# Kernel tuning notes

Measured on AMD Instinct MI355X. Metric: run time of the kernel, lower is better.

The kernel has to match this reference:

```python
import jax, jax.numpy as jnp
import numpy as np

B, N = 1, 1024
C_S, C_Z, N_HEAD, C_HEAD = 384, 128, 16, 24
HC = N_HEAD * C_HEAD


def _ln(x, eps=1e-5):
    m = jnp.mean(x, axis=-1, keepdims=True)
    v = jnp.var(x, axis=-1, keepdims=True)
    return (x - m) / jnp.sqrt(v + eps)


def setup_inputs() -> dict:
    key = jax.random.key(0)
    ks = jax.random.split(key, 24)
    w = lambda k, shp: (jax.random.normal(k, shp, jnp.float32) * 0.02)
    return {
        "a_i": jax.random.normal(ks[0], (B, N, C_S), jnp.float32),
        "s_i": jax.random.normal(ks[1], (B, N, C_S), jnp.float32),
        "z_ij": jax.random.normal(ks[2], (B, N, N, C_Z), jnp.float32),
        # AdaLN params
        "adaln_lns_w": jnp.ones((C_S,), jnp.float32),      # layer_norm_s weight (no bias)
        "adaln_ws": w(ks[3], (C_S, C_S)),                   # linear_s weight
        "adaln_bs": jnp.zeros((C_S,), jnp.float32),         # linear_s bias
        "adaln_wns": w(ks[4], (C_S, C_S)),                  # linear_no_bias_s
        # attention projections
        "wq": w(ks[5], (C_S, HC)),
        "bq": jnp.zeros((HC,), jnp.float32),
        "wk": w(ks[6], (C_S, HC)),
        "wv": w(ks[7], (C_S, HC)),
        # pair bias
        "lnb_w": jnp.ones((C_Z,), jnp.float32),
        "lnb_b": jnp.zeros((C_Z,), jnp.float32),
        "wb": w(ks[8], (C_Z, N_HEAD)),
        # gate + output
        "wg": w(ks[9], (C_S, HC)),
        "wo": w(ks[10], (HC, C_S)),
        # final conditioning gate (bias init -2.0 per module)
        "ws": w(ks[11], (C_S, C_S)),
        "bs": jnp.full((C_S,), -2.0, jnp.float32),
    }


def reference(a_i, s_i, z_ij, adaln_lns_w, adaln_ws, adaln_bs, adaln_wns,
              wq, bq, wk, wv, lnb_w, lnb_b, wb, wg, wo, ws, bs):
    b, n, _ = a_i.shape
    H, D = N_HEAD, C_HEAD
    # AdaLN: a <- sigmoid(Lin(s)) * LN(a) + Lin_nb(s)
    a = _ln(a_i)
    s = _ln(s_i) * adaln_lns_w
    a = jax.nn.sigmoid(s @ adaln_ws + adaln_bs) * a + s @ adaln_wns
    # QKV projections -> [b, i, h, d]
    q = (a @ wq + bq).reshape(b, n, H, D)
    k = (a @ wk).reshape(b, n, H, D)
    v = (a @ wv).reshape(b, n, H, D)
    # pair bias [b, h, i, j]
    bias = jnp.einsum('bijc,ch->bhij', _ln(z_ij) * lnb_w + lnb_b, wb)
    # gate [b, i, h, d]
    g = jax.nn.sigmoid(a @ wg).reshape(b, n, H, D)
    logits = jnp.einsum('bihd,bjhd->bhij', q, k) / jnp.sqrt(jnp.float32(D)) + bias
    A = jax.nn.softmax(logits, axis=-1)
    o = jnp.einsum('bhij,bjhd->bihd', A, v) * g
    o = o.reshape(b, n, H * D) @ wo
    # final gate uses raw s_i
    return jax.nn.sigmoid(s_i @ ws + bs) * o
```

## Files before the change

kernel.cpp:

```cpp
#include <hip/hip_runtime.h>
#include <hip/hip_bf16.h>
#include <math.h>

#define N_SEQ 1024
#define CS 384
#define CZ 128
#define NH 16
#define CH 24
#define HC 384

typedef float  floatx4 __attribute__((ext_vector_type(4)));
typedef short  shortx8 __attribute__((ext_vector_type(8)));
typedef unsigned int uintx4 __attribute__((ext_vector_type(4)));

__device__ __forceinline__ unsigned short f2bf(float f){
  union { float fv; unsigned u; } c; c.fv = f;
  unsigned u = c.u;
  return (unsigned short)((u + 0x7fffu + ((u >> 16) & 1u)) >> 16);
}
__device__ __forceinline__ float bf2f(unsigned short s){
  union { unsigned u; float fv; } c; c.u = ((unsigned)s) << 16; return c.fv;
}
__device__ __forceinline__ float bf_lo(unsigned u){
  union { unsigned uu; float f; } c; c.uu = u << 16; return c.f;
}
__device__ __forceinline__ float bf_hi(unsigned u){
  union { unsigned uu; float f; } c; c.uu = u & 0xffff0000u; return c.f;
}
__device__ __forceinline__ float sigmoidf_(float x){ return 1.f / (1.f + __expf(-x)); }

__device__ __forceinline__ void bias_unit(int u, int tid, int nthr,
    const float* __restrict__ z, const float* __restrict__ lnb_w,
    const float* __restrict__ lnb_b, const float* __restrict__ wb,
    unsigned short* __restrict__ bias, float (*ob)[65])
{
  int i    = u >> 4;
  int j0   = (u & 15) * 64;
  int wave = tid >> 6;
  int lane = tid & 63;

  if (wave < 4){
    int m = lane & 15;
    int q = lane >> 4;
    int jbase = j0 + wave * 16;

    shortx8 bfrag[4];
    float sumw = 0.f, sumb = 0.f;
    #pragma unroll
    for (int s = 0; s < 4; ++s){
      #pragma unroll
      for (int jj = 0; jj < 8; ++jj){
        int c = q*8 + jj + 32*s;
        float lw = lnb_w[c];
        float lb = lnb_b[c];
        float w  = wb[c*NH + m];
        bfrag[s][jj] = (short)f2bf(lw * w);
        sumw += lw * w;
        sumb += lb * w;
      }
    }
    sumw += __shfl_xor(sumw, 16); sumw += __shfl_xor(sumw, 32);
    sumb += __shfl_xor(sumb, 16); sumb += __shfl_xor(sumb, 32);

    const float* zrow = z + ((size_t)i * N_SEQ + (size_t)(jbase + m)) * CZ;
    floatx4 acc = {0.f, 0.f, 0.f, 0.f};
    float sum = 0.f, sq = 0.f;
    #pragma unroll
    for (int s = 0; s < 4; ++s){
      floatx4 z0 = *(const floatx4*)(zrow + q*8 + 32*s);
      floatx4 z1 = *(const floatx4*)(zrow + q*8 + 32*s + 4);
      shortx8 af;
      #pragma unroll
      for (int e = 0; e < 4; ++e){
        sum += z0[e]; sq += z0[e]*z0[e];
        sum += z1[e]; sq += z1[e]*z1[e];
        af[e]   = (short)f2bf(z0[e]);
        af[e+4] = (short)f2bf(z1[e]);
      }
      acc = __builtin_amdgcn_mfma_f32_16x16x32_bf16(af, bfrag[s], acc, 0, 0, 0);
    }
    sum += __shfl_xor(sum, 16); sum += __shfl_xor(sum, 32);
    sq  += __shfl_xor(sq , 16); sq  += __shfl_xor(sq , 32);
    float mean = sum * (1.f/CZ);
    float var  = sq  * (1.f/CZ) - mean*mean;
    float rstd = rsqrtf(var + 1e-5f);

    #pragma unroll
    for (int r = 0; r < 4; ++r){
      int row = q*4 + r;
      float mr = __shfl(mean, row);
      float rr = __shfl(rstd, row);
      ob[m][wave*16 + row] = rr * (acc[r] - mr * sumw) + sumb;
    }
  }
  __syncthreads();
  size_t base = (size_t)i * N_SEQ + j0;
  for (int idx = tid; idx < NH*64; idx += nthr){
    int hh = idx >> 6;
    int jj = idx & 63;
    bias[(size_t)hh * ((size_t)N_SEQ*N_SEQ) + base + jj] = f2bf(ob[hh][jj]);
  }
}

#define LN_BLOCKS 512
#define NB1 3072
__global__ __launch_bounds__(256) void ln_bias_kernel(
    const float* __restrict__ a_i, const float* __restrict__ s_i,
    const float* __restrict__ lns_w,
    float* __restrict__ a_ln, float* __restrict__ s_ln,
    const float* __restrict__ z, const float* __restrict__ lnb_w,
    const float* __restrict__ lnb_b, const float* __restrict__ wb,
    unsigned short* __restrict__ biasw)
{
  __shared__ float ob[NH][65];
  if (blockIdx.x >= LN_BLOCKS){
    bias_unit(blockIdx.x - LN_BLOCKS, threadIdx.x, 256, z, lnb_w, lnb_b, wb, biasw, ob);
    return;
  }
  float* red = &ob[0][0];
  int t    = threadIdx.x;
  int half = t >> 7;
  int tl   = t & 127;
  int row  = blockIdx.x*2 + half;
  float av[3], sv[3];
  float sa = 0.f, qa = 0.f, ss = 0.f, qs = 0.f;
  #pragma unroll
  for (int e = 0; e < 3; ++e){
    int c = tl + 128*e;
    float a = a_i[(size_t)row*CS + c];
    float s = s_i[(size_t)row*CS + c];
    av[e] = a; sv[e] = s;
    sa += a; qa += a*a; ss += s; qs += s*s;
  }
  #pragma unroll
  for (int off = 1; off < 64; off <<= 1){
    sa += __shfl_xor(sa, off);
    qa += __shfl_xor(qa, off);
    ss += __shfl_xor(ss, off);
    qs += __shfl_xor(qs, off);
  }
  if ((t & 63) == 0){
    int w = t >> 6;
    red[w*4+0] = sa; red[w*4+1] = qa; red[w*4+2] = ss; red[w*4+3] = qs;
  }
  __syncthreads();
  const float inv = 1.f / CS;
  int wb0 = half*2;
  float Sa = red[wb0*4+0] + red[(wb0+1)*4+0];
  float Qa = red[wb0*4+1] + red[(wb0+1)*4+1];
  float Ss = red[wb0*4+2] + red[(wb0+1)*4+2];
  float Qs = red[wb0*4+3] + red[(wb0+1)*4+3];
  float ma = Sa*inv, va = Qa*inv - ma*ma, ra = rsqrtf(va + 1e-5f);
  float ms = Ss*inv, vs = Qs*inv - ms*ms, rs = rsqrtf(vs + 1e-5f);
  #pragma unroll
  for (int e = 0; e < 3; ++e){
    int c = tl + 128*e;
    a_ln[(size_t)row*CS + c] = (av[e] - ma) * ra;
    s_ln[(size_t)row*CS + c] = (sv[e] - ms) * rs * lns_w[c];
  }
}

#define NB2 6656
__global__ __launch_bounds__(384) void adaln_bias_kernel(
    const float* __restrict__ X, const float* __restrict__ W1,
    const float* __restrict__ B1, const float* __restrict__ W2,
    const float* __restrict__ extra, float* __restrict__ OUT,
    const float* __restrict__ z, const float* __restrict__ lnb_w,
    const float* __restrict__ lnb_b, const float* __restrict__ wb,
    unsigned short* __restrict__ biasw)
{
  __shared__ float xl[4][CS];
  if (blockIdx.x >= 256){
    float (*ob)[65] = reinterpret_cast<float(*)[65]>(&xl[0][0]);
    bias_unit(NB1 + (blockIdx.x - 256), threadIdx.x, 384, z, lnb_w, lnb_b, wb, biasw, ob);
    return;
  }
  int r0 = blockIdx.x * 4;
  int t  = threadIdx.x;
  int ct = t % 96;
  int rg = t / 96;
  int c0 = ct * 4;
  #pragma unroll
  for (int rr = 0; rr < 4; ++rr)
    xl[rr][t] = X[(size_t)(r0+rr)*CS + t];
  __syncthreads();
  float acc1[4] = {0.f,0.f,0.f,0.f};
  float acc2[4] = {0.f,0.f,0.f,0.f};
  for (int k = 0; k < CS; k += 4){
    floatx4 s4 = *(const floatx4*)&xl[rg][k];
    #pragma unroll
    for (int kk = 0; kk < 4; ++kk){
      floatx4 w1 = *(const floatx4*)&W1[(size_t)(k+kk)*CS + c0];
      floatx4 w2 = *(const floatx4*)&W2[(size_t)(k+kk)*CS + c0];
      #pragma unroll
      for (int cc = 0; cc < 4; ++cc){
        acc1[cc] += s4[kk] * w1[cc];
        acc2[cc] += s4[kk] * w2[cc];
      }
    }
  }
  size_t obk = (size_t)(r0+rg) * CS + c0;
  #pragma unroll
  for (int cc = 0; cc < 4; ++cc)
    OUT[obk+cc] = sigmoidf_(acc1[cc] + B1[c0+cc]) * extra[obk+cc] + acc2[cc];
}

#define NB3 6656
__global__ __launch_bounds__(384) void qkvg_bias_kernel(
    const float* __restrict__ X,
    const float* __restrict__ wq, const float* __restrict__ bq,
    const float* __restrict__ wk, const float* __restrict__ wv,
    const float* __restrict__ wg,
    float* __restrict__ qo, float* __restrict__ ko,
    float* __restrict__ vo, float* __restrict__ go,
    const float* __restrict__ z, const float* __restrict__ lnb_w,
    const float* __restrict__ lnb_b, const float* __restrict__ wb,
    unsigned short* __restrict__ biasw)
{
  __shared__ float xl[4][CS];
  if (blockIdx.x >= 256){
    float (*ob)[65] = reinterpret_cast<float(*)[65]>(&xl[0][0]);
    bias_unit(NB1 + NB2 + (blockIdx.x - 256), threadIdx.x, 384, z, lnb_w, lnb_b, wb, biasw, ob);
    return;
  }
  int r0 = blockIdx.x * 4;
  int t  = threadIdx.x;
  int ct = t % 96;
  int rg = t / 96;
  int c0 = ct * 4;
  #pragma unroll
  for (int rr = 0; rr < 4; ++rr)
    xl[rr][t] = X[(size_t)(r0+rr)*CS + t];
  __syncthreads();
  float aq[4] = {0.f,0.f,0.f,0.f};
  float ak[4] = {0.f,0.f,0.f,0.f};
  float av4[4] = {0.f,0.f,0.f,0.f};
  float ag[4] = {0.f,0.f,0.f,0.f};
  for (int k = 0; k < CS; k += 4){
    floatx4 s4 = *(const floatx4*)&xl[rg][k];
    #pragma unroll
    for (int kk = 0; kk < 4; ++kk){
      floatx4 wq4 = *(const floatx4*)&wq[(size_t)(k+kk)*HC + c0];
      floatx4 wk4 = *(const floatx4*)&wk[(size_t)(k+kk)*HC + c0];
      floatx4 wv4 = *(const floatx4*)&wv[(size_t)(k+kk)*HC + c0];
      floatx4 wg4 = *(const floatx4*)&wg[(size_t)(k+kk)*HC + c0];
      #pragma unroll
      for (int cc = 0; cc < 4; ++cc){
        aq[cc]  += s4[kk] * wq4[cc];
        ak[cc]  += s4[kk] * wk4[cc];
        av4[cc] += s4[kk] * wv4[cc];
        ag[cc]  += s4[kk] * wg4[cc];
      }
    }
  }
  size_t obk = (size_t)(r0+rg) * HC + c0;
  #pragma unroll
  for (int cc = 0; cc < 4; ++cc){
    qo[obk+cc] = aq[cc] + bq[c0+cc];
    ko[obk+cc] = ak[cc];
    vo[obk+cc] = av4[cc];
    go[obk+cc] = sigmoidf_(ag[cc]);
  }
}

#define TJ 128
#define KROW 20
__global__ __launch_bounds__(256) void attn_kernel(
    const float* __restrict__ qq, const float* __restrict__ kk,
    const float* __restrict__ vv, const float* __restrict__ gg,
    const unsigned short* __restrict__ bias, float* __restrict__ att)
{
  int h  = blockIdx.x & 15;
  int i0 = (blockIdx.x >> 4) * 16;
  int il = threadIdx.x & 15;
  int jg = threadIdx.x >> 4;

  __shared__ unsigned int smem[TJ*KROW*2];

  float qr[24];
  {
    const float* qs = qq + (size_t)(i0+il)*CS + h*CH;
    #pragma unroll
    for (int e = 0; e < 6; ++e){
      floatx4 t4 = *(const floatx4*)(qs + 4*e);
      qr[4*e] = t4[0]; qr[4*e+1] = t4[1]; qr[4*e+2] = t4[2]; qr[4*e+3] = t4[3];
    }
  }
  const float scale = 0.20412414523193154f;
  float lrun = 0.f;
  float o[24];
  #pragma unroll
  for (int d = 0; d < 24; ++d) o[d] = 0.f;

  for (int jt = 0; jt < 8; ++jt){
    __syncthreads();
    {
      int row  = threadIdx.x >> 1;
      int half = threadIdx.x & 1;
      const float* ks = kk + (size_t)(jt*TJ + row)*CS + h*CH + half*12;
      const float* vs = vv + (size_t)(jt*TJ + row)*CS + h*CH + half*12;
      unsigned int* kd = smem + row*KROW + half*6;
      unsigned int* vd = smem + TJ*KROW + row*KROW + half*6;
      #pragma unroll
      for (int e = 0; e < 6; ++e){
        kd[e] = (unsigned)f2bf(ks[2*e]) | ((unsigned)f2bf(ks[2*e+1]) << 16);
        vd[e] = (unsigned)f2bf(vs[2*e]) | ((unsigned)f2bf(vs[2*e+1]) << 16);
      }
    }
    __syncthreads();
    const unsigned short* bptr = bias + (size_t)h*((size_t)N_SEQ*N_SEQ)
                               + (size_t)(i0+il)*N_SEQ + jt*TJ;
    #pragma unroll
    for (int tt = 0; tt < 8; ++tt){
      int jl = jg + 16*tt;
      uintx4 k0 = *(const uintx4*)&smem[jl*KROW];
      uintx4 k1 = *(const uintx4*)&smem[jl*KROW + 4];
      uintx4 k2 = *(const uintx4*)&smem[jl*KROW + 8];
      float dot = 0.f;
      #pragma unroll
      for (int e = 0; e < 4; ++e){
        dot += bf_lo(k0[e])*qr[2*e]      + bf_hi(k0[e])*qr[2*e+1];
        dot += bf_lo(k1[e])*qr[8+2*e]    + bf_hi(k1[e])*qr[8+2*e+1];
        dot += bf_lo(k2[e])*qr[16+2*e]   + bf_hi(k2[e])*qr[16+2*e+1];
      }
      float p = __expf(dot * scale + bf2f(bptr[jl]));
      lrun += p;
      uintx4 v0 = *(const uintx4*)&smem[TJ*KROW + jl*KROW];
      uintx4 v1 = *(const uintx4*)&smem[TJ*KROW + jl*KROW + 4];
      uintx4 v2 = *(const uintx4*)&smem[TJ*KROW + jl*KROW + 8];
      #pragma unroll
      for (int e = 0; e < 4; ++e){
        o[2*e]      += p * bf_lo(v0[e]);  o[2*e+1]    += p * bf_hi(v0[e]);
        o[8+2*e]    += p * bf_lo(v1[e]);  o[8+2*e+1]  += p * bf_hi(v1[e]);
        o[16+2*e]   += p * bf_lo(v2[e]);  o[16+2*e+1] += p * bf_hi(v2[e]);
      }
    }
  }
  __syncthreads();
  #pragma unroll
  for (int d = 0; d < 24; ++d){
    o[d] += __shfl_xor(o[d], 16);
    o[d] += __shfl_xor(o[d], 32);
  }
  lrun += __shfl_xor(lrun, 16);
  lrun += __shfl_xor(lrun, 32);
  float* mgf = (float*)smem;
  int lane = threadIdx.x & 63;
  int w    = threadIdx.x >> 6;
  if (lane < 16){
    float* slot = mgf + (w*16 + lane)*25;
    slot[0] = lrun;
    #pragma unroll
    for (int d = 0; d < 24; ++d) slot[1+d] = o[d];
  }
  __syncthreads();
  if (threadIdx.x < 16){
    int ii = threadIdx.x;
    float L = 0.f, O[24];
    #pragma unroll
    for (int d = 0; d < 24; ++d) O[d] = 0.f;
    for (int w2 = 0; w2 < 4; ++w2){
      const float* slot = mgf + (w2*16 + ii)*25;
      L += slot[0];
      #pragma unroll
      for (int d = 0; d < 24; ++d) O[d] += slot[1+d];
    }
    const float* gs = gg + (size_t)(i0+ii)*CS + h*CH;
    float* os = att + (size_t)(i0+ii)*CS + h*CH;
    float invL = 1.f / L;
    #pragma unroll
    for (int d = 0; d < 24; ++d) os[d] = O[d] * invL * gs[d];
  }
}

__global__ __launch_bounds__(384) void out_final_kernel(
    const float* __restrict__ attb, const float* __restrict__ wo,
    const float* __restrict__ s_i,  const float* __restrict__ wsm,
    const float* __restrict__ bsv,  float* __restrict__ out)
{
  __shared__ float xo[4][CS];
  __shared__ float xs[4][CS];
  int r0 = blockIdx.x * 4;
  int t  = threadIdx.x;
  int ct = t % 96;
  int rg = t / 96;
  int c0 = ct * 4;
  #pragma unroll
  for (int rr = 0; rr < 4; ++rr){
    xo[rr][t] = attb[(size_t)(r0+rr)*CS + t];
    xs[rr][t] = s_i [(size_t)(r0+rr)*CS + t];
  }
  __syncthreads();
  float ao[4] = {0.f,0.f,0.f,0.f};
  float as[4] = {0.f,0.f,0.f,0.f};
  for (int k = 0; k < CS; k += 4){
    floatx4 o4 = *(const floatx4*)&xo[rg][k];
    floatx4 s4 = *(const floatx4*)&xs[rg][k];
    #pragma unroll
    for (int kk = 0; kk < 4; ++kk){
      floatx4 w1 = *(const floatx4*)&wo [(size_t)(k+kk)*CS + c0];
      floatx4 w2 = *(const floatx4*)&wsm[(size_t)(k+kk)*CS + c0];
      #pragma unroll
      for (int cc = 0; cc < 4; ++cc){
        ao[cc] += o4[kk] * w1[cc];
        as[cc] += s4[kk] * w2[cc];
      }
    }
  }
  size_t obk = (size_t)(r0+rg) * CS + c0;
  #pragma unroll
  for (int cc = 0; cc < 4; ++cc)
    out[obk+cc] = sigmoidf_(as[cc] + bsv[c0+cc]) * ao[cc];
}

extern "C" void kernel_launch(void* const* d_in, const int* in_sizes, int n_in,
                              void* d_out, int out_size, void* d_ws, size_t ws_size,
                              hipStream_t stream) {
  const float* a_i     = (const float*)d_in[0];
  const float* s_i     = (const float*)d_in[1];
  const float* z_ij    = (const float*)d_in[2];
  const float* lns_w   = (const float*)d_in[3];
  const float* ada_ws  = (const float*)d_in[4];
  const float* ada_bs  = (const float*)d_in[5];
  const float* ada_wns = (const float*)d_in[6];
  const float* wq      = (const float*)d_in[7];
  const float* bq      = (const float*)d_in[8];
  const float* wk      = (const float*)d_in[9];
  const float* wv      = (const float*)d_in[10];
  const float* lnb_w   = (const float*)d_in[11];
  const float* lnb_b   = (const float*)d_in[12];
  const float* wb      = (const float*)d_in[13];
  const float* wg      = (const float*)d_in[14];
  const float* wo      = (const float*)d_in[15];
  const float* wsm     = (const float*)d_in[16];
  const float* bsv     = (const float*)d_in[17];

  const size_t RC = (size_t)N_SEQ * CS;
  float* wsf  = (float*)d_ws;
  float* s_ln = wsf;
  float* a_ln = wsf + RC;
  float* a    = wsf + 2*RC;
  float* qv   = wsf + 3*RC;
  float* kv   = wsf + 4*RC;
  float* vvp  = wsf + 5*RC;
  float* gv   = wsf + 6*RC;
  float* attb = wsf + 7*RC;
  unsigned short* biasw = (unsigned short*)(wsf + 9*RC);

  ln_bias_kernel<<<LN_BLOCKS + NB1, 256, 0, stream>>>(
      a_i, s_i, lns_w, a_ln, s_ln, z_ij, lnb_w, lnb_b, wb, biasw);
  adaln_bias_kernel<<<256 + NB2, 384, 0, stream>>>(
      s_ln, ada_ws, ada_bs, ada_wns, a_ln, a, z_ij, lnb_w, lnb_b, wb, biasw);
  qkvg_bias_kernel<<<256 + NB3, 384, 0, stream>>>(
      a, wq, bq, wk, wv, wg, qv, kv, vvp, gv, z_ij, lnb_w, lnb_b, wb, biasw);
  attn_kernel<<<N_SEQ, 256, 0, stream>>>(qv, kv, vvp, gv, biasw, attb);
  out_final_kernel<<<256, 384, 0, stream>>>(attb, wo, s_i, wsm, bsv, (float*)d_out);
}
```

Measured before the change: 1.060 ms.

## Fuse layer norms, AdaLN and QKVG projections into one pre-kernel with pair bias

Merges the three pre-attention kernels (LN, AdaLN GEMM, QKVG GEMM) into a single launch. Each block handles 8 rows kept in shared memory, so the intermediate a_ln, s_ln and a buffers never go to global memory. All pair-bias units now run in that one launch. The output GEMM also moves to 8 rows per block so each weight load serves two rows, and the attention kernel's K/V staging uses vector loads. The trade-off is fewer GEMM blocks (128), which may serialise the GEMM part behind the bias work in the combined grid.

```diff
diff --git a/kernel.cpp b/kernel.cpp
--- a/kernel.cpp
+++ b/kernel.cpp
@@ -26,6 +26,9 @@
 }
 __device__ __forceinline__ float bf_hi(unsigned u){
   union { unsigned uu; float f; } c; c.uu = u & 0xffff0000u; return c.f;
+}
+__device__ __forceinline__ unsigned pack2(float lo, float hi){
+  return (unsigned)f2bf(lo) | ((unsigned)f2bf(hi) << 16);
 }
 __device__ __forceinline__ float sigmoidf_(float x){ return 1.f / (1.f + __expf(-x)); }
 
@@ -102,112 +105,12 @@
   }
 }
 
-#define LN_BLOCKS 512
-#define NB1 3072
-__global__ __launch_bounds__(256) void ln_bias_kernel(
+#define NGEMM 128
+__global__ __launch_bounds__(384) void pre_kernel(
     const float* __restrict__ a_i, const float* __restrict__ s_i,
     const float* __restrict__ lns_w,
-    float* __restrict__ a_ln, float* __restrict__ s_ln,
-    const float* __restrict__ z, const float* __restrict__ lnb_w,
-    const float* __restrict__ lnb_b, const float* __restrict__ wb,
-    unsigned short* __restrict__ biasw)
-{
-  __shared__ float ob[NH][65];
-  if (blockIdx.x >= LN_BLOCKS){
-    bias_unit(blockIdx.x - LN_BLOCKS, threadIdx.x, 256, z, lnb_w, lnb_b, wb, biasw, ob);
-    return;
-  }
-  float* red = &ob[0][0];
-  int t    = threadIdx.x;
-  int half = t >> 7;
-  int tl   = t & 127;
-  int row  = blockIdx.x*2 + half;
-  float av[3], sv[3];
-  float sa = 0.f, qa = 0.f, ss = 0.f, qs = 0.f;
-  #pragma unroll
-  for (int e = 0; e < 3; ++e){
-    int c = tl + 128*e;
-    float a = a_i[(size_t)row*CS + c];
-    float s = s_i[(size_t)row*CS + c];
-    av[e] = a; sv[e] = s;
-    sa += a; qa += a*a; ss += s; qs += s*s;
-  }
-  #pragma unroll
-  for (int off = 1; off < 64; off <<= 1){
-    sa += __shfl_xor(sa, off);
-    qa += __shfl_xor(qa, off);
-    ss += __shfl_xor(ss, off);
-    qs += __shfl_xor(qs, off);
-  }
-  if ((t & 63) == 0){
-    int w = t >> 6;
-    red[w*4+0] = sa; red[w*4+1] = qa; red[w*4+2] = ss; red[w*4+3] = qs;
-  }
-  __syncthreads();
-  const float inv = 1.f / CS;
-  int wb0 = half*2;
-  float Sa = red[wb0*4+0] + red[(wb0+1)*4+0];
-  float Qa = red[wb0*4+1] + red[(wb0+1)*4+1];
-  float Ss = red[wb0*4+2] + red[(wb0+1)*4+2];
-  float Qs = red[wb0*4+3] + red[(wb0+1)*4+3];
-  float ma = Sa*inv, va = Qa*inv - ma*ma, ra = rsqrtf(va + 1e-5f);
-  float ms = Ss*inv, vs = Qs*inv - ms*ms, rs = rsqrtf(vs + 1e-5f);
-  #pragma unroll
-  for (int e = 0; e < 3; ++e){
-    int c = tl + 128*e;
-    a_ln[(size_t)row*CS + c] = (av[e] - ma) * ra;
-    s_ln[(size_t)row*CS + c] = (sv[e] - ms) * rs * lns_w[c];
-  }
-}
-
-#define NB2 6656
-__global__ __launch_bounds__(384) void adaln_bias_kernel(
-    const float* __restrict__ X, const float* __restrict__ W1,
-    const float* __restrict__ B1, const float* __restrict__ W2,
-    const float* __restrict__ extra, float* __restrict__ OUT,
-    const float* __restrict__ z, const float* __restrict__ lnb_w,
-    const float* __restrict__ lnb_b, const float* __restrict__ wb,
-    unsigned short* __restrict__ biasw)
-{
-  __shared__ float xl[4][CS];
-  if (blockIdx.x >= 256){
-    float (*ob)[65] = reinterpret_cast<float(*)[65]>(&xl[0][0]);
-    bias_unit(NB1 + (blockIdx.x - 256), threadIdx.x, 384, z, lnb_w, lnb_b, wb, biasw, ob);
-    return;
-  }
-  int r0 = blockIdx.x * 4;
-  int t  = threadIdx.x;
-  int ct = t % 96;
-  int rg = t / 96;
-  int c0 = ct * 4;
-  #pragma unroll
-  for (int rr = 0; rr < 4; ++rr)
-    xl[rr][t] = X[(size_t)(r0+rr)*CS + t];
-  __syncthreads();
-  float acc1[4] = {0.f,0.f,0.f,0.f};
-  float acc2[4] = {0.f,0.f,0.f,0.f};
-  for (int k = 0; k < CS; k += 4){
-    floatx4 s4 = *(const floatx4*)&xl[rg][k];
-    #pragma unroll
-    for (int kk = 0; kk < 4; ++kk){
-      floatx4 w1 = *(const floatx4*)&W1[(size_t)(k+kk)*CS + c0];
-      floatx4 w2 = *(const floatx4*)&W2[(size_t)(k+kk)*CS + c0];
-      #pragma unroll
-      for (int cc = 0; cc < 4; ++cc){
-        acc1[cc] += s4[kk] * w1[cc];
-        acc2[cc] += s4[kk] * w2[cc];
-      }
-    }
-  }
-  size_t obk = (size_t)(r0+rg) * CS + c0;
-  #pragma unroll
-  for (int cc = 0; cc < 4; ++cc)
-    OUT[obk+cc] = sigmoidf_(acc1[cc] + B1[c0+cc]) * extra[obk+cc] + acc2[cc];
-}
-
-#define NB3 6656
-__global__ __launch_bounds__(384) void qkvg_bias_kernel(
-    const float* __restrict__ X,
+    const float* __restrict__ W1, const float* __restrict__ B1,
+    const float* __restrict__ W2,
     const float* __restrict__ wq, const float* __restrict__ bq,
     const float* __restrict__ wk, const float* __restrict__ wv,
     const float* __restrict__ wg,
@@ -217,49 +120,127 @@
     const float* __restrict__ lnb_b, const float* __restrict__ wb,
     unsigned short* __restrict__ biasw)
 {
-  __shared__ float xl[4][CS];
-  if (blockIdx.x >= 256){
-    float (*ob)[65] = reinterpret_cast<float(*)[65]>(&xl[0][0]);
-    bias_unit(NB1 + NB2 + (blockIdx.x - 256), threadIdx.x, 384, z, lnb_w, lnb_b, wb, biasw, ob);
+  __shared__ float tileA[8][CS];
+  __shared__ float tileS[8][CS];
+  __shared__ float red[6][8][4];
+  __shared__ float fin[8][4];
+  if (blockIdx.x >= NGEMM){
+    bias_unit(blockIdx.x - NGEMM, threadIdx.x, 384, z, lnb_w, lnb_b, wb, biasw,
+              reinterpret_cast<float(*)[65]>(&tileA[0][0]));
     return;
   }
-  int r0 = blockIdx.x * 4;
+  int r0 = blockIdx.x * 8;
   int t  = threadIdx.x;
-  int ct = t % 96;
-  int rg = t / 96;
-  int c0 = ct * 4;
-  #pragma unroll
-  for (int rr = 0; rr < 4; ++rr)
-    xl[rr][t] = X[(size_t)(r0+rr)*CS + t];
-  __syncthreads();
-  float aq[4] = {0.f,0.f,0.f,0.f};
-  float ak[4] = {0.f,0.f,0.f,0.f};
-  float av4[4] = {0.f,0.f,0.f,0.f};
-  float ag[4] = {0.f,0.f,0.f,0.f};
-  for (int k = 0; k < CS; k += 4){
-    floatx4 s4 = *(const floatx4*)&xl[rg][k];
-    #pragma unroll
-    for (int kk = 0; kk < 4; ++kk){
-      floatx4 wq4 = *(const floatx4*)&wq[(size_t)(k+kk)*HC + c0];
-      floatx4 wk4 = *(const floatx4*)&wk[(size_t)(k+kk)*HC + c0];
-      floatx4 wv4 = *(const floatx4*)&wv[(size_t)(k+kk)*HC + c0];
-      floatx4 wg4 = *(const floatx4*)&wg[(size_t)(k+kk)*HC + c0];
-      #pragma unroll
-      for (int cc = 0; cc < 4; ++cc){
-        aq[cc]  += s4[kk] * wq4[cc];
-        ak[cc]  += s4[kk] * wk4[cc];
-        av4[cc] += s4[kk] * wv4[cc];
-        ag[cc]  += s4[kk] * wg4[cc];
-      }
-    }
-  }
-  size_t obk = (size_t)(r0+rg) * HC + c0;
-  #pragma unroll
-  for (int cc = 0; cc < 4; ++cc){
-    qo[obk+cc] = aq[cc] + bq[c0+cc];
-    ko[obk+cc] = ak[cc];
-    vo[obk+cc] = av4[cc];
-    go[obk+cc] = sigmoidf_(ag[cc]);
+  float sa[8], qa[8], ss[8], qs[8];
+  #pragma unroll
+  for (int rr = 0; rr < 8; ++rr){
+    float a = a_i[(size_t)(r0+rr)*CS + t];
+    float s = s_i[(size_t)(r0+rr)*CS + t];
+    tileA[rr][t] = a; tileS[rr][t] = s;
+    sa[rr] = a; qa[rr] = a*a; ss[rr] = s; qs[rr] = s*s;
+  }
+  #pragma unroll
+  for (int rr = 0; rr < 8; ++rr){
+    #pragma unroll
+    for (int off = 1; off < 64; off <<= 1){
+      sa[rr] += __shfl_xor(sa[rr], off);
+      qa[rr] += __shfl_xor(qa[rr], off);
+      ss[rr] += __shfl_xor(ss[rr], off);
+      qs[rr] += __shfl_xor(qs[rr], off);
+    }
+  }
+  {
+    int lane = t & 63, w = t >> 6;
+    if (lane == 0){
+      #pragma unroll
+      for (int rr = 0; rr < 8; ++rr){
+        red[w][rr][0]=sa[rr]; red[w][rr][1]=qa[rr];
+        red[w][rr][2]=ss[rr]; red[w][rr][3]=qs[rr];
+      }
+    }
+  }
+  __syncthreads();
+  if (t < 8){
+    float Sa=0.f,Qa=0.f,Ss=0.f,Qs=0.f;
+    #pragma unroll
+    for (int w=0; w<6; ++w){
+      Sa+=red[w][t][0]; Qa+=red[w][t][1]; Ss+=red[w][t][2]; Qs+=red[w][t][3];
+    }
+    const float inv = 1.f/CS;
+    float ma=Sa*inv, va=Qa*inv-ma*ma;
+    float ms=Ss*inv, vs=Qs*inv-ms*ms;
+    fin[t][0]=ma; fin[t][1]=rsqrtf(va+1e-5f);
+    fin[t][2]=ms; fin[t][3]=rsqrtf(vs+1e-5f);
+  }
+  __syncthreads();
+  {
+    float lw = lns_w[t];
+    #pragma unroll
+    for (int rr = 0; rr < 8; ++rr){
+      tileA[rr][t] = (tileA[rr][t]-fin[rr][0])*fin[rr][1];
+      tileS[rr][t] = (tileS[rr][t]-fin[rr][2])*fin[rr][3]*lw;
+    }
+  }
+  __syncthreads();
+  int ct = t % 96, rgg = t / 96, c0 = ct*4;
+  {
+    float A1[2][4]={{0.f}}, A2[2][4]={{0.f}};
+    for (int k=0;k<CS;k+=4){
+      floatx4 xa = *(const floatx4*)&tileS[rgg][k];
+      floatx4 xb = *(const floatx4*)&tileS[rgg+4][k];
+      #pragma unroll
+      for (int kk=0;kk<4;++kk){
+        floatx4 w1 = *(const floatx4*)&W1[(size_t)(k+kk)*CS + c0];
+        floatx4 w2 = *(const floatx4*)&W2[(size_t)(k+kk)*CS + c0];
+        #pragma unroll
+        for (int cc=0;cc<4;++cc){
+          A1[0][cc] += xa[kk]*w1[cc];  A1[1][cc] += xb[kk]*w1[cc];
+          A2[0][cc] += xa[kk]*w2[cc];  A2[1][cc] += xb[kk]*w2[cc];
+        }
+      }
+    }
+    #pragma unroll
+    for (int r2=0;r2<2;++r2){
+      int rr = rgg + 4*r2;
+      #pragma unroll
+      for (int cc=0;cc<4;++cc){
+        float g = sigmoidf_(A1[r2][cc] + B1[c0+cc]);
+        tileA[rr][c0+cc] = g * tileA[rr][c0+cc] + A2[r2][cc];
+      }
+    }
+  }
+  __syncthreads();
+  {
+    float AQ[2][4]={{0.f}}, AK[2][4]={{0.f}}, AV[2][4]={{0.f}}, AG[2][4]={{0.f}};
+    for (int k=0;k<CS;k+=4){
+      floatx4 xa = *(const floatx4*)&tileA[rgg][k];
+      floatx4 xb = *(const floatx4*)&tileA[rgg+4][k];
+      #pragma unroll
+      for (int kk=0;kk<4;++kk){
+        floatx4 q4 = *(const floatx4*)&wq[(size_t)(k+kk)*HC + c0];
+        floatx4 k4 = *(const floatx4*)&wk[(size_t)(k+kk)*HC + c0];
+        floatx4 v4 = *(const floatx4*)&wv[(size_t)(k+kk)*HC + c0];
+        floatx4 g4 = *(const floatx4*)&wg[(size_t)(k+kk)*HC + c0];
+        #pragma unroll
+        for (int cc=0;cc<4;++cc){
+          AQ[0][cc]+=xa[kk]*q4[cc]; AQ[1][cc]+=xb[kk]*q4[cc];
+          AK[0][cc]+=xa[kk]*k4[cc]; AK[1][cc]+=xb[kk]*k4[cc];
+          AV[0][cc]+=xa[kk]*v4[cc]; AV[1][cc]+=xb[kk]*v4[cc];
+          AG[0][cc]+=xa[kk]*g4[cc]; AG[1][cc]+=xb[kk]*g4[cc];
+        }
+      }
+    }
+    #pragma unroll
+    for (int r2=0;r2<2;++r2){
+      size_t ob = (size_t)(r0 + rgg + 4*r2)*HC + c0;
+      #pragma unroll
+      for (int cc=0;cc<4;++cc){
+        qo[ob+cc] = AQ[r2][cc] + bq[c0+cc];
+        ko[ob+cc] = AK[r2][cc];
+        vo[ob+cc] = AV[r2][cc];
+        go[ob+cc] = sigmoidf_(AG[r2][cc]);
+      }
+    }
   }
 }
 
@@ -299,13 +280,20 @@
       int half = threadIdx.x & 1;
       const float* ks = kk + (size_t)(jt*TJ + row)*CS + h*CH + half*12;
       const float* vs = vv + (size_t)(jt*TJ + row)*CS + h*CH + half*12;
+      floatx4 a0 = *(const floatx4*)(ks);
+      floatx4 a1 = *(const floatx4*)(ks+4);
+      floatx4 a2 = *(const floatx4*)(ks+8);
+      floatx4 b0 = *(const floatx4*)(vs);
+      floatx4 b1 = *(const floatx4*)(vs+4);
+      floatx4 b2 = *(const floatx4*)(vs+8);
       unsigned int* kd = smem + row*KROW + half*6;
       unsigned int* vd = smem + TJ*KROW + row*KROW + half*6;
-      #pragma unroll
-      for (int e = 0; e < 6; ++e){
-        kd[e] = (unsigned)f2bf(ks[2*e]) | ((unsigned)f2bf(ks[2*e+1]) << 16);
-        vd[e] = (unsigned)f2bf(vs[2*e]) | ((unsigned)f2bf(vs[2*e+1]) << 16);
-      }
+      kd[0]=pack2(a0[0],a0[1]); kd[1]=pack2(a0[2],a0[3]);
+      kd[2]=pack2(a1[0],a1[1]); kd[3]=pack2(a1[2],a1[3]);
+      kd[4]=pack2(a2[0],a2[1]); kd[5]=pack2(a2[2],a2[3]);
+      vd[0]=pack2(b0[0],b0[1]); vd[1]=pack2(b0[2],b0[3]);
+      vd[2]=pack2(b1[0],b1[1]); vd[3]=pack2(b1[2],b1[3]);
+      vd[4]=pack2(b2[0],b2[1]); vd[5]=pack2(b2[2],b2[3]);
     }
     __syncthreads();
     const unsigned short* bptr = bias + (size_t)h*((size_t)N_SEQ*N_SEQ)
@@ -378,39 +366,41 @@
     const float* __restrict__ s_i,  const float* __restrict__ wsm,
     const float* __restrict__ bsv,  float* __restrict__ out)
 {
-  __shared__ float xo[4][CS];
-  __shared__ float xs[4][CS];
-  int r0 = blockIdx.x * 4;
+  __shared__ float xo[8][CS];
+  __shared__ float xs[8][CS];
+  int r0 = blockIdx.x * 8;
   int t  = threadIdx.x;
-  int ct = t % 96;
-  int rg = t / 96;
-  int c0 = ct * 4;
-  #pragma unroll
-  for (int rr = 0; rr < 4; ++rr){
+  #pragma unroll
+  for (int rr = 0; rr < 8; ++rr){
     xo[rr][t] = attb[(size_t)(r0+rr)*CS + t];
     xs[rr][t] = s_i [(size_t)(r0+rr)*CS + t];
   }
   __syncthreads();
-  float ao[4] = {0.f,0.f,0.f,0.f};
-  float as[4] = {0.f,0.f,0.f,0.f};
-  for (int k = 0; k < CS; k += 4){
-    floatx4 o4 = *(const floatx4*)&xo[rg][k];
-    floatx4 s4 = *(const floatx4*)&xs[rg][k];
-    #pragma unroll
-    for (int kk = 0; kk < 4; ++kk){
+  int ct = t % 96, rgg = t / 96, c0 = ct*4;
+  float AO[2][4]={{0.f}}, AS[2][4]={{0.f}};
+  for (int k=0;k<CS;k+=4){
+    floatx4 oa = *(const floatx4*)&xo[rgg][k];
+    floatx4 ob4 = *(const floatx4*)&xo[rgg+4][k];
+    floatx4 sa4 = *(const floatx4*)&xs[rgg][k];
+    floatx4 sb4 = *(const floatx4*)&xs[rgg+4][k];
+    #pragma unroll
+    for (int kk=0;kk<4;++kk){
       floatx4 w1 = *(const floatx4*)&wo [(size_t)(k+kk)*CS + c0];
       floatx4 w2 = *(const floatx4*)&wsm[(size_t)(k+kk)*CS + c0];
       #pragma unroll
-      for (int cc = 0; cc < 4; ++cc){
-        ao[cc] += o4[kk] * w1[cc];
-        as[cc] += s4[kk] * w2[cc];
-      }
-    }
-  }
-  size_t obk = (size_t)(r0+rg) * CS + c0;
-  #pragma unroll
-  for (int cc = 0; cc < 4; ++cc)
-    out[obk+cc] = sigmoidf_(as[cc] + bsv[c0+cc]) * ao[cc];
+      for (int cc=0;cc<4;++cc){
+        AO[0][cc] += oa[kk]*w1[cc];  AO[1][cc] += ob4[kk]*w1[cc];
+        AS[0][cc] += sa4[kk]*w2[cc]; AS[1][cc] += sb4[kk]*w2[cc];
+      }
+    }
+  }
+  #pragma unroll
+  for (int r2=0;r2<2;++r2){
+    size_t ob = (size_t)(r0 + rgg + 4*r2)*CS + c0;
+    #pragma unroll
+    for (int cc=0;cc<4;++cc)
+      out[ob+cc] = sigmoidf_(AS[r2][cc] + bsv[c0+cc]) * AO[r2][cc];
+  }
 }
 
 extern "C" void kernel_launch(void* const* d_in, const int* in_sizes, int n_in,
@@ -437,9 +427,6 @@
 
   const size_t RC = (size_t)N_SEQ * CS;
   float* wsf  = (float*)d_ws;
-  float* s_ln = wsf;
-  float* a_ln = wsf + RC;
-  float* a    = wsf + 2*RC;
   float* qv   = wsf + 3*RC;
   float* kv   = wsf + 4*RC;
   float* vvp  = wsf + 5*RC;
@@ -447,12 +434,10 @@
   float* attb = wsf + 7*RC;
   unsigned short* biasw = (unsigned short*)(wsf + 9*RC);
 
-  ln_bias_kernel<<<LN_BLOCKS + NB1, 256, 0, stream>>>(
-      a_i, s_i, lns_w, a_ln, s_ln, z_ij, lnb_w, lnb_b, wb, biasw);
-  adaln_bias_kernel<<<256 + NB2, 384, 0, stream>>>(
-      s_ln, ada_ws, ada_bs, ada_wns, a_ln, a, z_ij, lnb_w, lnb_b, wb, biasw);
-  qkvg_bias_kernel<<<256 + NB3, 384, 0, stream>>>(
-      a, wq, bq, wk, wv, wg, qv, kv, vvp, gv, z_ij, lnb_w, lnb_b, wb, biasw);
+  pre_kernel<<<NGEMM + N_SEQ*16, 384, 0, stream>>>(
+      a_i, s_i, lns_w, ada_ws, ada_bs, ada_wns,
+      wq, bq, wk, wv, wg, qv, kv, vvp, gv,
+      z_ij, lnb_w, lnb_b, wb, biasw);
   attn_kernel<<<N_SEQ, 256, 0, stream>>>(qv, kv, vvp, gv, biasw, attb);
-  out_final_kernel<<<256, 384, 0, stream>>>(attb, wo, s_i, wsm, bsv, (float*)d_out);
-}
+  out_final_kernel<<<N_SEQ/8, 384, 0, stream>>>(attb, wo, s_i, wsm, bsv, (float*)d_out);
+}
```

Measured after the change: 1.038 ms. -2.1%, faster.
